# Performance work log

Hardware: AMD Instinct MI355X
Metric: run time of the kernel (lower is better)

Reference implementation:

```python
import jax, jax.numpy as jnp
import numpy as np

N_NODES = 50000      # nodes
N_EDGES = 800000     # edges (avg degree 16)
D = 128              # input_dim == hidden_dim
C = 32               # output_dim (classes)
G = 64               # number of graphs in batch
EPS = 1e-5           # LayerNorm eps (torch default)
NUM_LAYERS = 3


def setup_inputs() -> dict:
    key = jax.random.key(0)
    ks = jax.random.split(key, 12)
    scale = 1.0 / np.sqrt(D)
    x = jax.random.normal(ks[0], (N_NODES, D), dtype=jnp.float32)
    edge_index = jax.random.randint(ks[1], (2, N_EDGES), 0, N_NODES)
    batch = jnp.sort(jax.random.randint(ks[2], (N_NODES,), 0, G))
    # CustomConv params: self-loop linear + message linear, 3 layers stacked
    W_self = jax.random.normal(ks[3], (NUM_LAYERS, D, D), dtype=jnp.float32) * scale
    b_self = jnp.zeros((NUM_LAYERS, D), dtype=jnp.float32)
    W_msg = jax.random.normal(ks[4], (NUM_LAYERS, D, D), dtype=jnp.float32) * scale
    b_msg = jnp.zeros((NUM_LAYERS, D), dtype=jnp.float32)
    # two LayerNorms (after layers 0 and 1)
    ln_g = jnp.ones((2, D), dtype=jnp.float32)
    ln_b = jnp.zeros((2, D), dtype=jnp.float32)
    # post-MP MLP head: Linear(D,D) -> Dropout(identity in eval) -> Linear(D,C)
    W1 = jax.random.normal(ks[5], (D, D), dtype=jnp.float32) * scale
    b1 = jnp.zeros((D,), dtype=jnp.float32)
    W2 = jax.random.normal(ks[6], (D, C), dtype=jnp.float32) * scale
    b2 = jnp.zeros((C,), dtype=jnp.float32)
    return {"x": x, "W_self": W_self, "b_self": b_self, "W_msg": W_msg,
            "b_msg": b_msg, "ln_g": ln_g, "ln_b": ln_b, "W1": W1, "b1": b1,
            "W2": W2, "b2": b2, "edge_index": edge_index, "batch": batch}


def _layer_norm(h, g, b):
    mu = jnp.mean(h, axis=-1, keepdims=True)
    var = jnp.mean(jnp.square(h - mu), axis=-1, keepdims=True)
    return g * (h - mu) * jax.lax.rsqrt(var + EPS) + b


def reference(x, W_self, b_self, W_msg, b_msg, ln_g, ln_b, W1, b1, W2, b2,
              edge_index, batch):
    src, dst = edge_index[0], edge_index[1]
    for i in range(NUM_LAYERS):
        # CustomConv: self linear + sum-aggregated neighbor messages
        msg = x @ W_msg[i] + b_msg[i]                     # [N, D]
        agg = jax.ops.segment_sum(msg[src], dst, num_segments=N_NODES)
        x = x @ W_self[i] + b_self[i] + agg               # [N, D]
        x = jax.nn.relu(x)
        # dropout p=0.25 is identity in eval mode
        if i != NUM_LAYERS - 1:
            x = _layer_norm(x, ln_g[i], ln_b[i])
    # global mean pool over graphs
    sums = jax.ops.segment_sum(x, batch, num_segments=G)          # [G, D]
    cnt = jax.ops.segment_sum(jnp.ones((N_NODES,), x.dtype), batch,
                              num_segments=G)                     # [G]
    pooled = sums / jnp.maximum(cnt, 1.0)[:, None]
    # post-MP head (dropout identity in eval)
    h = pooled @ W1 + b1
    logits = h @ W2 + b2                                          # [G, C]
    return jax.nn.log_softmax(logits, axis=1)
```

## Files before the change

kernel.cpp:

```cpp
#include <hip/hip_runtime.h>
#include <hip/hip_bf16.h>
#include <math.h>

#define N_NODES 50000
#define N_EDGES 800000
#define DIM 128
#define CLS 32
#define NGRAPH 64
#define LN_EPS 1e-5f
#define CSR_CAP (N_EDGES + 8 * N_NODES)
#define NBLK 196
#define ABLK 128
#define EPB (N_EDGES / ABLK)
#define EB_STRIDE 7168
#define LCAP 8192
#define PSPLIT 16
#define ROWS1 (N_NODES + 1)

typedef __attribute__((ext_vector_type(8))) short bf16x8;
typedef __attribute__((ext_vector_type(4))) float f32x4;

static __device__ __forceinline__ int lower_bound_i(const int* a, int n, int key) {
    int lo = 0, hi = n;
    while (lo < hi) { int mid = (lo + hi) >> 1; if (a[mid] < key) lo = mid + 1; else hi = mid; }
    return lo;
}


__global__ __launch_bounds__(256) void prep_kernel(
    const float* __restrict__ x, const float* __restrict__ Wself,
    const float* __restrict__ Wmsg, __hip_bfloat16* __restrict__ XbIn,
    __hip_bfloat16* __restrict__ WT,
    int* __restrict__ ecur, float* __restrict__ gsum,
    __hip_bfloat16* __restrict__ padA, __hip_bfloat16* __restrict__ padB,
    __hip_bfloat16* __restrict__ padC) {
    int i = blockIdx.x * 256 + threadIdx.x;
    if (i < N_NODES * DIM / 2) {
        float2 v = ((const float2*)x)[i];
        ((__hip_bfloat162*)XbIn)[i] = __float22bfloat162_rn(v);
    }
    if (i < 3 * 128 * 256) {
        int l = i / (128 * 256);
        int rem = i - l * (128 * 256);
        int n = rem >> 8;
        int k = rem & 255;
        float v = (k < 128) ? Wself[l * 16384 + k * 128 + n]
                            : Wmsg[l * 16384 + (k - 128) * 128 + n];
        WT[i] = __float2bfloat16(v);
    }
    if (i < NBLK) ecur[i] = i * EB_STRIDE;
    if (i < NGRAPH * DIM) gsum[i] = 0.f;
    if (i < DIM) {
        padA[i] = __float2bfloat16(0.f);
        padB[i] = __float2bfloat16(0.f);
        padC[i] = __float2bfloat16(0.f);
    }
}


__global__ __launch_bounds__(1024) void bucket_kernel(
    const int* __restrict__ esrc, const int* __restrict__ edst,
    int* __restrict__ ecur, int* __restrict__ ebuf) {
    __shared__ int bc[NBLK], bres[NBLK], bcnt[NBLK];
    const int t = threadIdx.x;
    const int e0 = blockIdx.x * EPB;
    if (t < NBLK) bc[t] = 0;
    __syncthreads();
    for (int i = t; i < EPB; i += 1024)
        atomicAdd(&bc[edst[e0 + i] >> 8], 1);
    __syncthreads();
    if (t < NBLK) {
        int c = bc[t];
        int r = (c + 15) & ~15;
        int res = atomicAdd(&ecur[t], r);
        bres[t] = res;
        bcnt[t] = c;
        bc[t] = res;
    }
    __syncthreads();
    for (int i = t; i < EPB; i += 1024) {
        int d = edst[e0 + i];
        int s = esrc[e0 + i];
        int pos = atomicAdd(&bc[d >> 8], 1);
        ebuf[pos] = ((d & 255) << 16) | s;
    }
    __syncthreads();
    if (t < NBLK) {
        int c = bcnt[t], r = (c + 15) & ~15, base = bres[t];
        for (int j = c; j < r; j++) ebuf[base + j] = -1;
    }
}


__global__ __launch_bounds__(1024) void bhist_kernel(
    const int* __restrict__ ebuf, const int* __restrict__ ecur,
    int* __restrict__ counts, int* __restrict__ btot) {
    __shared__ int ncnt[256];
    __shared__ int red[256];
    const int b = blockIdx.x, t = threadIdx.x;
    const int used = ecur[b] - b * EB_STRIDE;
    const int* eb = ebuf + b * EB_STRIDE;
    if (t < 256) ncnt[t] = 0;
    __syncthreads();
    for (int i = t; i < used; i += 1024) {
        int p = eb[i];
        if (p != -1) atomicAdd(&ncnt[p >> 16], 1);
    }
    __syncthreads();
    if (t < 256) {
        int gi = b * 256 + t;
        if (gi < N_NODES) counts[gi] = ncnt[t];
        red[t] = (ncnt[t] + 7) & ~7;
    }
    __syncthreads();
    for (int o = 128; o > 0; o >>= 1) {
        if (t < o) red[t] += red[t + o];
        __syncthreads();
    }
    if (t == 0) btot[b] = red[0];
}


__global__ __launch_bounds__(256) void btot_scan_kernel(const int* __restrict__ btot,
                                                        int* __restrict__ bbase,
                                                        int* __restrict__ off) {
    __shared__ int sd[256];
    int i = threadIdx.x;
    int v = (i < NBLK) ? btot[i] : 0;
    sd[i] = v;
    __syncthreads();
    for (int o = 1; o < 256; o <<= 1) {
        int tv = (i >= o) ? sd[i - o] : 0;
        __syncthreads();
        sd[i] += tv;
        __syncthreads();
    }
    if (i < NBLK) bbase[i] = sd[i] - v;
    if (i == 255) off[N_NODES] = sd[255];
}


__global__ __launch_bounds__(1024) void csr_build_kernel(
    const int* __restrict__ ebuf, const int* __restrict__ ecur,
    const int* __restrict__ counts, const int* __restrict__ bbase,
    int* __restrict__ off, int* __restrict__ csr) {
    __shared__ int cur[256];
    __shared__ int ssc[256];
    __shared__ int lcsr[LCAP];
    const int b = blockIdx.x, t = threadIdx.x;
    const int used = ecur[b] - b * EB_STRIDE;
    const int* eb = ebuf + b * EB_STRIDE;
    const int gbase = bbase[b];
    for (int i = t; i < LCAP; i += 1024) lcsr[i] = N_NODES;
    int myc = 0, mypad = 0;
    const int gi = b * 256 + t;
    if (t < 256) {
        myc = (gi < N_NODES) ? counts[gi] : 0;
        mypad = (myc + 7) & ~7;
        ssc[t] = mypad;
    }
    __syncthreads();
    for (int o = 1; o < 256; o <<= 1) {
        int v = 0;
        if (t < 256 && t >= o) v = ssc[t - o];
        __syncthreads();
        if (t < 256) ssc[t] += v;
        __syncthreads();
    }
    if (t < 256) {
        int eoff = ssc[t] - mypad;
        cur[t] = eoff;
        if (gi < N_NODES) off[gi] = gbase + eoff;
    }
    __syncthreads();
    for (int i = t; i < used; i += 1024) {
        int p = eb[i];
        if (p != -1) {
            int pos = atomicAdd(&cur[p >> 16], 1);
            lcsr[pos] = p & 0xFFFF;
        }
    }
    __syncthreads();
    const int total = ssc[255];
    int4* dst4 = (int4*)(csr + gbase);
    const int4* src4 = (const int4*)lcsr;
    for (int i = t; i < (total >> 2); i += 1024) dst4[i] = src4[i];
}


__global__ __launch_bounds__(256) void agg_kernel(const __hip_bfloat16* __restrict__ Xb,
                                                  const int* __restrict__ off,
                                                  const int* __restrict__ csr,
                                                  __hip_bfloat16* __restrict__ Sb) {
    const int wave = threadIdx.x >> 6;
    const int lane = threadIdx.x & 63;
    const int n = blockIdx.x * 4 + wave;
    if (n >= N_NODES) return;
    const int seg = lane >> 4;
    const int cl = lane & 15;
    int b = off[n], e = off[n + 1];
    float ac[8];
#pragma unroll
    for (int j = 0; j < 8; j++) ac[j] = 0.f;
    int base = b;
    for (; base + 16 <= e; base += 16) {
        int idx16 = csr[base + (lane & 15)];
        int s[4];
        uint4 v[4];
#pragma unroll
        for (int r = 0; r < 4; r++) s[r] = __shfl(idx16, r * 4 + seg, 64);
#pragma unroll
        for (int r = 0; r < 4; r++)
            v[r] = *(const uint4*)(Xb + (size_t)s[r] * DIM + cl * 8);
#pragma unroll
        for (int r = 0; r < 4; r++) {
            unsigned int u[4] = {v[r].x, v[r].y, v[r].z, v[r].w};
#pragma unroll
            for (int k = 0; k < 4; k++) {
                union { unsigned int b32; float f; } lo, hi;
                lo.b32 = u[k] << 16;
                hi.b32 = u[k] & 0xffff0000u;
                ac[2 * k] += lo.f;
                ac[2 * k + 1] += hi.f;
            }
        }
    }
    if (base < e) {
        int idx8 = csr[base + (lane & 7)];
        int s0 = __shfl(idx8, seg, 64);
        int s1 = __shfl(idx8, 4 + seg, 64);
        uint4 v0 = *(const uint4*)(Xb + (size_t)s0 * DIM + cl * 8);
        uint4 v1 = *(const uint4*)(Xb + (size_t)s1 * DIM + cl * 8);
        unsigned int u[8] = {v0.x, v0.y, v0.z, v0.w, v1.x, v1.y, v1.z, v1.w};
#pragma unroll
        for (int k = 0; k < 8; k++) {
            union { unsigned int b32; float f; } lo, hi;
            lo.b32 = u[k] << 16;
            hi.b32 = u[k] & 0xffff0000u;
            ac[2 * (k & 3)] += lo.f;
            ac[2 * (k & 3) + 1] += hi.f;
        }
    }
#pragma unroll
    for (int j = 0; j < 8; j++) {
        ac[j] += __shfl_xor(ac[j], 16, 64);
        ac[j] += __shfl_xor(ac[j], 32, 64);
    }
    if (lane < 16) {
        union { uint4 u; __hip_bfloat162 h[4]; } pk;
#pragma unroll
        for (int k = 0; k < 4; k++)
            pk.h[k] = __float22bfloat162_rn(make_float2(ac[2 * k], ac[2 * k + 1]));
        *(uint4*)(Sb + (size_t)n * DIM + cl * 8) = pk.u;
    }
}


__global__ __launch_bounds__(256) void layer_mfma_kernel(
    const __hip_bfloat16* __restrict__ Xb, const __hip_bfloat16* __restrict__ Sb,
    const __hip_bfloat16* __restrict__ WT,
    const float* __restrict__ bself, const float* __restrict__ bmsg,
    const int* __restrict__ deg,
    const float* __restrict__ lng, const float* __restrict__ lnb,
    __hip_bfloat16* __restrict__ XoutB, int do_ln) {
    __shared__ __hip_bfloat16 wlds[128 * 136];
    const int tid = threadIdx.x;
    const int w = tid >> 6, lane = tid & 63;
    const int l15 = lane & 15, q = lane >> 4;

    const int row = blockIdx.x * 64 + w * 16 + l15;
    const int rowc = min(row, N_NODES);

    f32x4 acc[8];
#pragma unroll
    for (int ct = 0; ct < 8; ct++) acc[ct] = (f32x4){0.f, 0.f, 0.f, 0.f};

    const __hip_bfloat16* Abase[2] = {Xb, Sb};
    for (int c = 0; c < 2; c++) {
        __syncthreads();
        {
            int n = tid >> 1, h = tid & 1;
            const uint4* src = (const uint4*)(WT + n * 256 + c * 128 + h * 64);
            uint4* dst = (uint4*)(&wlds[n * 136 + h * 64]);
#pragma unroll
            for (int i = 0; i < 8; i++) dst[i] = src[i];
        }
        __syncthreads();
        const __hip_bfloat16* arow = Abase[c] + (size_t)rowc * DIM;
#pragma unroll
        for (int ks = 0; ks < 4; ks++) {
            bf16x8 afrag = *(const bf16x8*)(arow + ks * 32 + q * 8);
#pragma unroll
            for (int ct = 0; ct < 8; ct++) {
                bf16x8 bfrag = *(const bf16x8*)(&wlds[(ct * 16 + l15) * 136 + ks * 32 + q * 8]);
                acc[ct] = __builtin_amdgcn_mfma_f32_16x16x32_bf16(afrag, bfrag, acc[ct], 0, 0, 0);
            }
        }
    }

    const int growbase = blockIdx.x * 64 + w * 16;
#pragma unroll
    for (int r = 0; r < 4; r++) {
        int grow = growbase + q * 4 + r;
        bool valid = grow < N_NODES;
        float dg = valid ? (float)deg[grow] : 0.f;
        float v[8];
        float s1 = 0.f;
#pragma unroll
        for (int ct = 0; ct < 8; ct++) {
            int col = ct * 16 + l15;
            float h = acc[ct][r] + bself[col] + dg * bmsg[col];
            h = fmaxf(h, 0.f);
            v[ct] = h;
            s1 += h;
        }
        if (do_ln) {
#pragma unroll
            for (int m = 1; m < 16; m <<= 1) s1 += __shfl_xor(s1, m, 64);
            float mu = s1 * (1.0f / 128.0f);
            float s2 = 0.f;
#pragma unroll
            for (int ct = 0; ct < 8; ct++) { float d = v[ct] - mu; s2 += d * d; }
#pragma unroll
            for (int m = 1; m < 16; m <<= 1) s2 += __shfl_xor(s2, m, 64);
            float rs = rsqrtf(s2 * (1.0f / 128.0f) + LN_EPS);
#pragma unroll
            for (int ct = 0; ct < 8; ct++) {
                int col = ct * 16 + l15;
                v[ct] = lng[col] * (v[ct] - mu) * rs + lnb[col];
            }
        }
        if (valid) {
#pragma unroll
            for (int ct = 0; ct < 8; ct++) {
                int col = ct * 16 + l15;
                XoutB[(size_t)grow * DIM + col] = __float2bfloat16(v[ct]);
            }
        }
    }
}


__global__ __launch_bounds__(128) void pool_partial_kernel(const __hip_bfloat16* __restrict__ X,
                                                           const int* __restrict__ batch,
                                                           float* __restrict__ gsum) {
    int g = blockIdx.x;
    int s = blockIdx.y;
    int lo = lower_bound_i(batch, N_NODES, g);
    int hi = lower_bound_i(batch, N_NODES, g + 1);
    int len = hi - lo;
    int a = lo + (int)(((long long)len * s) / PSPLIT);
    int b = lo + (int)(((long long)len * (s + 1)) / PSPLIT);
    int c = threadIdx.x;
    float acc = 0.f;
    for (int n = a; n < b; n++) acc += __bfloat162float(X[(size_t)n * DIM + c]);
    if (b > a) atomicAdd(&gsum[g * DIM + c], acc);
}

__global__ __launch_bounds__(128) void head_kernel(
    const float* __restrict__ gsum, const int* __restrict__ batch,
    const float* __restrict__ W1, const float* __restrict__ b1,
    const float* __restrict__ W2, const float* __restrict__ b2,
    float* __restrict__ out) {
    __shared__ float p[128];
    __shared__ float hh[128];
    int g = blockIdx.x;
    int j = threadIdx.x;
    int lo = lower_bound_i(batch, N_NODES, g);
    int hi = lower_bound_i(batch, N_NODES, g + 1);
    float cnt = fmaxf((float)(hi - lo), 1.0f);
    p[j] = gsum[g * DIM + j] / cnt;
    __syncthreads();
    float s = b1[j];
    for (int k = 0; k < DIM; k++) s += p[k] * W1[k * DIM + j];
    hh[j] = s;
    __syncthreads();
    if (j < CLS) {
        float l = b2[j];
        for (int k = 0; k < DIM; k++) l += hh[k] * W2[k * CLS + j];
        float mx = l;
#pragma unroll
        for (int m = 16; m >= 1; m >>= 1) mx = fmaxf(mx, __shfl_xor(mx, m, 64));
        float ex = expf(l - mx);
        float se = ex;
#pragma unroll
        for (int m = 16; m >= 1; m >>= 1) se += __shfl_xor(se, m, 64);
        out[g * CLS + j] = l - mx - logf(se);
    }
}


extern "C" void kernel_launch(void* const* d_in, const int* in_sizes, int n_in,
                              void* d_out, int out_size, void* d_ws, size_t ws_size,
                              hipStream_t stream) {
    (void)in_sizes; (void)n_in; (void)out_size; (void)ws_size;
    const float* x     = (const float*)d_in[0];
    const float* Wself = (const float*)d_in[1];
    const float* bself = (const float*)d_in[2];
    const float* Wmsg  = (const float*)d_in[3];
    const float* bmsg  = (const float*)d_in[4];
    const float* lng   = (const float*)d_in[5];
    const float* lnb   = (const float*)d_in[6];
    const float* W1    = (const float*)d_in[7];
    const float* b1    = (const float*)d_in[8];
    const float* W2    = (const float*)d_in[9];
    const float* b2    = (const float*)d_in[10];
    const int*   ei    = (const int*)d_in[11];
    const int*   batch = (const int*)d_in[12];
    const int* esrc = ei;
    const int* edst = ei + N_EDGES;

    char* w = (char*)d_ws;
    size_t o = 0;
    auto alloc = [&](size_t bytes) { void* p = w + o; o += (bytes + 255) & ~(size_t)255; return p; };
    __hip_bfloat16* XbIn = (__hip_bfloat16*)alloc((size_t)ROWS1 * DIM * 2);
    __hip_bfloat16* Xb0  = (__hip_bfloat16*)alloc((size_t)ROWS1 * DIM * 2);
    __hip_bfloat16* Xb1  = (__hip_bfloat16*)alloc((size_t)ROWS1 * DIM * 2);
    __hip_bfloat16* Sb   = (__hip_bfloat16*)alloc((size_t)ROWS1 * DIM * 2);
    __hip_bfloat16* WT   = (__hip_bfloat16*)alloc((size_t)3 * 128 * 256 * 2);
    int*   counts = (int*)alloc((size_t)N_NODES * 4);
    int*   offs   = (int*)alloc((size_t)(N_NODES + 1) * 4);
    int*   btot   = (int*)alloc((size_t)NBLK * 4);
    int*   bbase  = (int*)alloc((size_t)NBLK * 4);
    int*   ecur   = (int*)alloc((size_t)NBLK * 4);
    int*   ebuf   = (int*)alloc((size_t)NBLK * EB_STRIDE * 4);
    int*   csr    = (int*)alloc((size_t)CSR_CAP * 4);
    float* gsum   = (float*)alloc((size_t)NGRAPH * DIM * 4);

    prep_kernel<<<(N_NODES * DIM / 2 + 255) / 256, 256, 0, stream>>>(
        x, Wself, Wmsg, XbIn, WT, ecur, gsum,
        XbIn + (size_t)N_NODES * DIM, Xb0 + (size_t)N_NODES * DIM,
        Xb1 + (size_t)N_NODES * DIM);
    hipMemsetAsync(Sb + (size_t)N_NODES * DIM, 0, DIM * 2, stream);

    bucket_kernel<<<ABLK, 1024, 0, stream>>>(esrc, edst, ecur, ebuf);
    bhist_kernel<<<NBLK, 1024, 0, stream>>>(ebuf, ecur, counts, btot);
    btot_scan_kernel<<<1, 256, 0, stream>>>(btot, bbase, offs);
    csr_build_kernel<<<NBLK, 1024, 0, stream>>>(ebuf, ecur, counts, bbase, offs, csr);

    const __hip_bfloat16* XbCur = XbIn;
    __hip_bfloat16* bbufs[3] = {Xb0, Xb1, Xb0};
    for (int i = 0; i < 3; i++) {
        agg_kernel<<<(N_NODES + 3) / 4, 256, 0, stream>>>(XbCur, offs, csr, Sb);
        layer_mfma_kernel<<<(N_NODES + 63) / 64, 256, 0, stream>>>(
            XbCur, Sb, WT + (size_t)i * 128 * 256,
            bself + i * DIM, bmsg + i * DIM, counts,
            (i < 2) ? lng + i * DIM : lng, (i < 2) ? lnb + i * DIM : lnb,
            bbufs[i], (i < 2) ? 1 : 0);
        XbCur = bbufs[i];
    }

    pool_partial_kernel<<<dim3(NGRAPH, PSPLIT), 128, 0, stream>>>(bbufs[2], batch, gsum);
    head_kernel<<<NGRAPH, 128, 0, stream>>>(gsum, batch, W1, b1, W2, b2, (float*)d_out);
}
```

Measured before the change: 290.8 us.

## Fuse CSR build passes, use per-block CSR slots, and fuse pooling into last layer

Merges the histogram, block-total scan and CSR build kernels into one kernel. Each destination block now writes its CSR into a fixed LCAP-sized slot instead of a globally scanned offset, so agg reads node end offsets from padded counts. Global mean-pool accumulation moves into the final layer GEMM epilogue with wave-level reduction plus atomics, and the separate pool kernel is dropped. Bucketing uses more blocks with replicated shared histograms and register-cached edges, and the Sb pad memset is folded into prep.

```diff
diff --git a/kernel.cpp b/kernel.cpp
--- a/kernel.cpp
+++ b/kernel.cpp
@@ -8,13 +8,11 @@
 #define CLS 32
 #define NGRAPH 64
 #define LN_EPS 1e-5f
-#define CSR_CAP (N_EDGES + 8 * N_NODES)
 #define NBLK 196
-#define ABLK 128
+#define ABLK 256
 #define EPB (N_EDGES / ABLK)
 #define EB_STRIDE 7168
 #define LCAP 8192
-#define PSPLIT 16
 #define ROWS1 (N_NODES + 1)
 
 typedef __attribute__((ext_vector_type(8))) short bf16x8;
@@ -33,7 +31,7 @@
     __hip_bfloat16* __restrict__ WT,
     int* __restrict__ ecur, float* __restrict__ gsum,
     __hip_bfloat16* __restrict__ padA, __hip_bfloat16* __restrict__ padB,
-    __hip_bfloat16* __restrict__ padC) {
+    __hip_bfloat16* __restrict__ padC, __hip_bfloat16* __restrict__ padD) {
     int i = blockIdx.x * 256 + threadIdx.x;
     if (i < N_NODES * DIM / 2) {
         float2 v = ((const float2*)x)[i];
@@ -54,6 +52,7 @@
         padA[i] = __float2bfloat16(0.f);
         padB[i] = __float2bfloat16(0.f);
         padC[i] = __float2bfloat16(0.f);
+        padD[i] = __float2bfloat16(0.f);
     }
 }
 
@@ -61,101 +60,70 @@
 __global__ __launch_bounds__(1024) void bucket_kernel(
     const int* __restrict__ esrc, const int* __restrict__ edst,
     int* __restrict__ ecur, int* __restrict__ ebuf) {
+    __shared__ int bc4[4][NBLK];
     __shared__ int bc[NBLK], bres[NBLK], bcnt[NBLK];
     const int t = threadIdx.x;
     const int e0 = blockIdx.x * EPB;
-    if (t < NBLK) bc[t] = 0;
-    __syncthreads();
-    for (int i = t; i < EPB; i += 1024)
-        atomicAdd(&bc[edst[e0 + i] >> 8], 1);
+    for (int i = t; i < 4 * NBLK; i += 1024) ((int*)bc4)[i] = 0;
+    __syncthreads();
+    int dr[4], sr[4];
+#pragma unroll
+    for (int it = 0; it < 4; it++) {
+        int i = t + it * 1024;
+        if (i < EPB) { dr[it] = edst[e0 + i]; sr[it] = esrc[e0 + i]; }
+        else { dr[it] = -1; sr[it] = 0; }
+    }
+    const int cpy = (t >> 6) & 3;
+#pragma unroll
+    for (int it = 0; it < 4; it++)
+        if (dr[it] >= 0) atomicAdd(&bc4[cpy][dr[it] >> 8], 1);
     __syncthreads();
     if (t < NBLK) {
-        int c = bc[t];
-        int r = (c + 15) & ~15;
+        int c = bc4[0][t] + bc4[1][t] + bc4[2][t] + bc4[3][t];
+        int r = (c + 7) & ~7;
         int res = atomicAdd(&ecur[t], r);
         bres[t] = res;
         bcnt[t] = c;
         bc[t] = res;
     }
     __syncthreads();
-    for (int i = t; i < EPB; i += 1024) {
-        int d = edst[e0 + i];
-        int s = esrc[e0 + i];
-        int pos = atomicAdd(&bc[d >> 8], 1);
-        ebuf[pos] = ((d & 255) << 16) | s;
-    }
+#pragma unroll
+    for (int it = 0; it < 4; it++)
+        if (dr[it] >= 0) {
+            int d = dr[it];
+            int pos = atomicAdd(&bc[d >> 8], 1);
+            ebuf[pos] = ((d & 255) << 16) | sr[it];
+        }
     __syncthreads();
     if (t < NBLK) {
-        int c = bcnt[t], r = (c + 15) & ~15, base = bres[t];
+        int c = bcnt[t], r = (c + 7) & ~7, base = bres[t];
         for (int j = c; j < r; j++) ebuf[base + j] = -1;
     }
 }
 
 
-__global__ __launch_bounds__(1024) void bhist_kernel(
+__global__ __launch_bounds__(1024) void csr_fused_kernel(
     const int* __restrict__ ebuf, const int* __restrict__ ecur,
-    int* __restrict__ counts, int* __restrict__ btot) {
+    int* __restrict__ counts, int* __restrict__ off, int* __restrict__ csr) {
     __shared__ int ncnt[256];
-    __shared__ int red[256];
-    const int b = blockIdx.x, t = threadIdx.x;
-    const int used = ecur[b] - b * EB_STRIDE;
-    const int* eb = ebuf + b * EB_STRIDE;
-    if (t < 256) ncnt[t] = 0;
-    __syncthreads();
-    for (int i = t; i < used; i += 1024) {
-        int p = eb[i];
-        if (p != -1) atomicAdd(&ncnt[p >> 16], 1);
-    }
-    __syncthreads();
-    if (t < 256) {
-        int gi = b * 256 + t;
-        if (gi < N_NODES) counts[gi] = ncnt[t];
-        red[t] = (ncnt[t] + 7) & ~7;
-    }
-    __syncthreads();
-    for (int o = 128; o > 0; o >>= 1) {
-        if (t < o) red[t] += red[t + o];
-        __syncthreads();
-    }
-    if (t == 0) btot[b] = red[0];
-}
-
-
-__global__ __launch_bounds__(256) void btot_scan_kernel(const int* __restrict__ btot,
-                                                        int* __restrict__ bbase,
-                                                        int* __restrict__ off) {
-    __shared__ int sd[256];
-    int i = threadIdx.x;
-    int v = (i < NBLK) ? btot[i] : 0;
-    sd[i] = v;
-    __syncthreads();
-    for (int o = 1; o < 256; o <<= 1) {
-        int tv = (i >= o) ? sd[i - o] : 0;
-        __syncthreads();
-        sd[i] += tv;
-        __syncthreads();
-    }
-    if (i < NBLK) bbase[i] = sd[i] - v;
-    if (i == 255) off[N_NODES] = sd[255];
-}
-
-
-__global__ __launch_bounds__(1024) void csr_build_kernel(
-    const int* __restrict__ ebuf, const int* __restrict__ ecur,
-    const int* __restrict__ counts, const int* __restrict__ bbase,
-    int* __restrict__ off, int* __restrict__ csr) {
+    __shared__ int ssc[256];
     __shared__ int cur[256];
-    __shared__ int ssc[256];
     __shared__ int lcsr[LCAP];
     const int b = blockIdx.x, t = threadIdx.x;
     const int used = ecur[b] - b * EB_STRIDE;
     const int* eb = ebuf + b * EB_STRIDE;
-    const int gbase = bbase[b];
     for (int i = t; i < LCAP; i += 1024) lcsr[i] = N_NODES;
+    if (t < 256) ncnt[t] = 0;
+    __syncthreads();
+    for (int i = t; i < used; i += 1024) {
+        int p = eb[i];
+        if (p != -1) atomicAdd(&ncnt[p >> 16], 1);
+    }
+    __syncthreads();
     int myc = 0, mypad = 0;
     const int gi = b * 256 + t;
     if (t < 256) {
-        myc = (gi < N_NODES) ? counts[gi] : 0;
+        myc = (gi < N_NODES) ? ncnt[t] : 0;
         mypad = (myc + 7) & ~7;
         ssc[t] = mypad;
     }
@@ -170,7 +138,10 @@
     if (t < 256) {
         int eoff = ssc[t] - mypad;
         cur[t] = eoff;
-        if (gi < N_NODES) off[gi] = gbase + eoff;
+        if (gi < N_NODES) {
+            off[gi] = b * LCAP + eoff;
+            counts[gi] = myc;
+        }
     }
     __syncthreads();
     for (int i = t; i < used; i += 1024) {
@@ -182,7 +153,7 @@
     }
     __syncthreads();
     const int total = ssc[255];
-    int4* dst4 = (int4*)(csr + gbase);
+    int4* dst4 = (int4*)(csr + b * LCAP);
     const int4* src4 = (const int4*)lcsr;
     for (int i = t; i < (total >> 2); i += 1024) dst4[i] = src4[i];
 }
@@ -190,6 +161,7 @@
 
 __global__ __launch_bounds__(256) void agg_kernel(const __hip_bfloat16* __restrict__ Xb,
                                                   const int* __restrict__ off,
+                                                  const int* __restrict__ counts,
                                                   const int* __restrict__ csr,
                                                   __hip_bfloat16* __restrict__ Sb) {
     const int wave = threadIdx.x >> 6;
@@ -198,7 +170,8 @@
     if (n >= N_NODES) return;
     const int seg = lane >> 4;
     const int cl = lane & 15;
-    int b = off[n], e = off[n + 1];
+    int b = off[n];
+    int e = b + ((counts[n] + 7) & ~7);
     float ac[8];
 #pragma unroll
     for (int j = 0; j < 8; j++) ac[j] = 0.f;
@@ -262,7 +235,8 @@
     const float* __restrict__ bself, const float* __restrict__ bmsg,
     const int* __restrict__ deg,
     const float* __restrict__ lng, const float* __restrict__ lnb,
-    __hip_bfloat16* __restrict__ XoutB, int do_ln) {
+    const int* __restrict__ batch, float* __restrict__ gsum,
+    __hip_bfloat16* __restrict__ XoutB, int do_ln, int do_pool) {
     __shared__ __hip_bfloat16 wlds[128 * 136];
     const int tid = threadIdx.x;
     const int w = tid >> 6, lane = tid & 63;
@@ -299,6 +273,17 @@
     }
 
     const int growbase = blockIdx.x * 64 + w * 16;
+    float racc[8];
+#pragma unroll
+    for (int ct = 0; ct < 8; ct++) racc[ct] = 0.f;
+    int gw = 0;
+    bool fastp = false;
+    if (do_pool) {
+        int first = (growbase < N_NODES) ? growbase : (N_NODES - 1);
+        gw = batch[first];
+        int lastrow = growbase + 15;
+        fastp = (growbase < N_NODES) && (lastrow < N_NODES) && (batch[lastrow] == gw);
+    }
 #pragma unroll
     for (int r = 0; r < 4; r++) {
         int grow = growbase + q * 4 + r;
@@ -330,7 +315,17 @@
                 v[ct] = lng[col] * (v[ct] - mu) * rs + lnb[col];
             }
         }
-        if (valid) {
+        if (do_pool) {
+            if (fastp) {
+#pragma unroll
+                for (int ct = 0; ct < 8; ct++) racc[ct] += v[ct];
+            } else if (valid) {
+                int g = batch[grow];
+#pragma unroll
+                for (int ct = 0; ct < 8; ct++)
+                    atomicAdd(&gsum[g * DIM + ct * 16 + l15], v[ct]);
+            }
+        } else if (valid) {
 #pragma unroll
             for (int ct = 0; ct < 8; ct++) {
                 int col = ct * 16 + l15;
@@ -338,24 +333,20 @@
             }
         }
     }
-}
-
-
-__global__ __launch_bounds__(128) void pool_partial_kernel(const __hip_bfloat16* __restrict__ X,
-                                                           const int* __restrict__ batch,
-                                                           float* __restrict__ gsum) {
-    int g = blockIdx.x;
-    int s = blockIdx.y;
-    int lo = lower_bound_i(batch, N_NODES, g);
-    int hi = lower_bound_i(batch, N_NODES, g + 1);
-    int len = hi - lo;
-    int a = lo + (int)(((long long)len * s) / PSPLIT);
-    int b = lo + (int)(((long long)len * (s + 1)) / PSPLIT);
-    int c = threadIdx.x;
-    float acc = 0.f;
-    for (int n = a; n < b; n++) acc += __bfloat162float(X[(size_t)n * DIM + c]);
-    if (b > a) atomicAdd(&gsum[g * DIM + c], acc);
-}
+    if (do_pool && fastp) {
+#pragma unroll
+        for (int ct = 0; ct < 8; ct++) {
+            racc[ct] += __shfl_xor(racc[ct], 16, 64);
+            racc[ct] += __shfl_xor(racc[ct], 32, 64);
+        }
+        if (q == 0) {
+#pragma unroll
+            for (int ct = 0; ct < 8; ct++)
+                atomicAdd(&gsum[gw * DIM + ct * 16 + l15], racc[ct]);
+        }
+    }
+}
+
 
 __global__ __launch_bounds__(128) void head_kernel(
     const float* __restrict__ gsum, const int* __restrict__ batch,
@@ -420,36 +411,31 @@
     __hip_bfloat16* WT   = (__hip_bfloat16*)alloc((size_t)3 * 128 * 256 * 2);
     int*   counts = (int*)alloc((size_t)N_NODES * 4);
     int*   offs   = (int*)alloc((size_t)(N_NODES + 1) * 4);
-    int*   btot   = (int*)alloc((size_t)NBLK * 4);
-    int*   bbase  = (int*)alloc((size_t)NBLK * 4);
     int*   ecur   = (int*)alloc((size_t)NBLK * 4);
     int*   ebuf   = (int*)alloc((size_t)NBLK * EB_STRIDE * 4);
-    int*   csr    = (int*)alloc((size_t)CSR_CAP * 4);
+    int*   csr    = (int*)alloc((size_t)NBLK * LCAP * 4);
     float* gsum   = (float*)alloc((size_t)NGRAPH * DIM * 4);
 
     prep_kernel<<<(N_NODES * DIM / 2 + 255) / 256, 256, 0, stream>>>(
         x, Wself, Wmsg, XbIn, WT, ecur, gsum,
         XbIn + (size_t)N_NODES * DIM, Xb0 + (size_t)N_NODES * DIM,
-        Xb1 + (size_t)N_NODES * DIM);
-    hipMemsetAsync(Sb + (size_t)N_NODES * DIM, 0, DIM * 2, stream);
+        Xb1 + (size_t)N_NODES * DIM, Sb + (size_t)N_NODES * DIM);
 
     bucket_kernel<<<ABLK, 1024, 0, stream>>>(esrc, edst, ecur, ebuf);
-    bhist_kernel<<<NBLK, 1024, 0, stream>>>(ebuf, ecur, counts, btot);
-    btot_scan_kernel<<<1, 256, 0, stream>>>(btot, bbase, offs);
-    csr_build_kernel<<<NBLK, 1024, 0, stream>>>(ebuf, ecur, counts, bbase, offs, csr);
+    csr_fused_kernel<<<NBLK, 1024, 0, stream>>>(ebuf, ecur, counts, offs, csr);
 
     const __hip_bfloat16* XbCur = XbIn;
     __hip_bfloat16* bbufs[3] = {Xb0, Xb1, Xb0};
     for (int i = 0; i < 3; i++) {
-        agg_kernel<<<(N_NODES + 3) / 4, 256, 0, stream>>>(XbCur, offs, csr, Sb);
+        agg_kernel<<<(N_NODES + 3) / 4, 256, 0, stream>>>(XbCur, offs, counts, csr, Sb);
         layer_mfma_kernel<<<(N_NODES + 63) / 64, 256, 0, stream>>>(
             XbCur, Sb, WT + (size_t)i * 128 * 256,
             bself + i * DIM, bmsg + i * DIM, counts,
             (i < 2) ? lng + i * DIM : lng, (i < 2) ? lnb + i * DIM : lnb,
-            bbufs[i], (i < 2) ? 1 : 0);
+            batch, gsum,
+            bbufs[i], (i < 2) ? 1 : 0, (i == 2) ? 1 : 0);
         XbCur = bbufs[i];
     }
 
-    pool_partial_kernel<<<dim3(NGRAPH, PSPLIT), 128, 0, stream>>>(bbufs[2], batch, gsum);
     head_kernel<<<NGRAPH, 128, 0, stream>>>(gsum, batch, W1, b1, W2, b2, (float*)d_out);
 }
```

Result: faster. 263.1 us (-9.5%).
